# Kernel optimization log

Hardware: AMD Instinct MI355X
Metric: run time of the kernel (lower is better)

## Reference

```python
import jax, jax.numpy as jnp
import numpy as np

N, D, E, L, NL = 100000, 64, 400000, 4, 10000
NEG = jnp.float32(-1e30)


def _make_graph(key):
    k1, k2, k3, k4 = jax.random.split(key, 4)
    ncov = N - NL
    # nodes [0, NL) never appear as source -> exactly NL leaves
    src_cov = jnp.arange(ncov, dtype=jnp.int32) + NL
    src_rand = jax.random.randint(k1, (E - ncov,), NL, N, dtype=jnp.int32)
    src = jnp.concatenate([src_cov, src_rand])
    dst = jax.random.randint(k2, (E,), 0, N, dtype=jnp.int32)
    edge_index = jnp.stack([src, dst])  # [2, E]
    edge_attr = jax.random.normal(k3, (E, D), jnp.float32)
    # partition edges into L 'topological level' masks
    edge_masks = (jnp.arange(E) % L)[None, :] == jnp.arange(L)[:, None]  # [L, E] bool
    x = jax.random.normal(k4, (N, D), jnp.float32)
    return x, edge_index, edge_attr, edge_masks


def setup_inputs() -> dict:
    key = jax.random.key(0)
    kg1, kg2, kp = jax.random.split(key, 3)
    x1, ei1, ea1, em1 = _make_graph(kg1)
    x2, ei2, ea2, em2 = _make_graph(kg2)
    ks = jax.random.split(kp, 10)
    s = 1.0 / np.sqrt(D)
    params = {
        'We': jax.random.normal(ks[0], (D, D), jnp.float32) * s,
        'be': jax.random.normal(ks[1], (D,), jnp.float32) * s,
        'Wa': jax.random.normal(ks[2], (1, 2 * D), jnp.float32) * s,
        'ba': jax.random.normal(ks[3], (1,), jnp.float32) * s,
        'Wih': jax.random.normal(ks[4], (3 * D, D), jnp.float32) * s,
        'Whh': jax.random.normal(ks[5], (3 * D, D), jnp.float32) * s,
        'bih': jax.random.normal(ks[6], (3 * D,), jnp.float32) * s,
        'bhh': jax.random.normal(ks[7], (3 * D,), jnp.float32) * s,
        'Wc': jax.random.normal(ks[8], (2 * D, 2 * D), jnp.float32) * s,
        'bc': jax.random.normal(ks[9], (2 * D,), jnp.float32) * s,
    }
    return dict(x1=x1, edge_index1=ei1, edge_attr1=ea1, edge_masks1=em1,
                x2=x2, edge_index2=ei2, edge_attr2=ea2, edge_masks2=em2,
                **params, n_leaf=NL)


def _gru(x, h, Wih, Whh, bih, bhh):
    # torch.nn.GRUCell math
    gi = x @ Wih.T + bih
    gh = h @ Whh.T + bhh
    ir, iz, in_ = jnp.split(gi, 3, axis=-1)
    hr, hz, hn = jnp.split(gh, 3, axis=-1)
    r = jax.nn.sigmoid(ir + hr)
    z = jax.nn.sigmoid(iz + hz)
    n = jnp.tanh(in_ + r * hn)
    return (1.0 - z) * n + z * h


def _flow_forward(x, edge_index, edge_attr, edge_masks,
                  We, be, Wa, ba, Wih, Whh, bih, bhh):
    Nn, Dm = x.shape
    src, dst = edge_index[0], edge_index[1]
    root = jnp.ones((Nn,), bool).at[dst].set(False)  # nodes with no incoming edge
    eemb = edge_attr @ We.T + be                     # [E, D] edge_lin
    # roots: GRU with zero hidden; others start at 0 (zeros_like in torch)
    h0 = jnp.where(root[:, None], _gru(x, jnp.zeros_like(x), Wih, Whh, bih, bhh), 0.0)
    q = x[dst]                                       # h_prev_i, level-invariant

    def step(h, mask):
        k = h[src] + eemb                            # h_j + edge_emb
        logit = (jnp.concatenate([q, k], axis=-1) @ Wa.T + ba)[:, 0]  # [E]
        ml = jnp.where(mask, logit, NEG)
        mx = jnp.maximum(jax.ops.segment_max(ml, dst, num_segments=Nn), NEG)
        ex = jnp.where(mask, jnp.exp(ml - mx[dst]), 0.0)  # scatter-softmax numerator
        den = jax.ops.segment_sum(ex, dst, num_segments=Nn)
        alpha = ex / (den[dst] + 1e-16)
        msg = jax.ops.segment_sum(alpha[:, None] * h[src], dst, num_segments=Nn)
        nm = jax.ops.segment_sum(mask.astype(jnp.float32), dst, num_segments=Nn) > 0
        h_new = _gru(x, msg, Wih, Whh, bih, bhh)     # input=h_prev, hidden=msg
        return jnp.where(nm[:, None], h_new, h), None

    h, _ = jax.lax.scan(step, h0, edge_masks)
    return h


def reference(x1, edge_index1, edge_attr1, edge_masks1,
              x2, edge_index2, edge_attr2, edge_masks2,
              We, be, Wa, ba, Wih, Whh, bih, bhh, Wc, bc, n_leaf):
    o1 = _flow_forward(x1, edge_index1, edge_attr1, edge_masks1,
                       We, be, Wa, ba, Wih, Whh, bih, bhh)
    o2 = _flow_forward(x2, edge_index2, edge_attr2, edge_masks2,
                       We, be, Wa, ba, Wih, Whh, bih, bhh)
    Dm = x1.shape[1]
    leaf1 = jnp.ones((x1.shape[0],), bool).at[edge_index1[0]].set(False)
    leaf2 = jnp.ones((x2.shape[0],), bool).at[edge_index2[0]].set(False)
    idx1 = jnp.nonzero(leaf1, size=n_leaf)[0]
    idx2 = jnp.nonzero(leaf2, size=n_leaf)[0]
    feat = jnp.concatenate([o1[idx1], o2[idx2]], axis=-1) @ Wc.T + bc  # [NL, 2D]
    o1 = o1.at[idx1].set(feat[:, :Dm])
    o2 = o2.at[idx2].set(feat[:, Dm:])
    return (o1, o2)
```

## Files before the change

### kernel.cpp

```cpp
#include <hip/hip_runtime.h>

#define NN 100000
#define DD 64
#define EE 400000
#define LL 4
#define NLEAF 10000
#define NT (2*NN)
#define ETOT (2*EE)
#define M4 (4*NT)
#define NBLK ((M4 + 1023)/1024)

typedef __attribute__((ext_vector_type(8))) short bf8v;
typedef __attribute__((ext_vector_type(4))) float f4v;

__device__ __forceinline__ float rcp_(float x){ return __builtin_amdgcn_rcpf(x); }
__device__ __forceinline__ float sigm_(float x){ return rcp_(1.f + __expf(-x)); }
__device__ __forceinline__ float tanh_(float x){
  x = fminf(fmaxf(x, -15.f), 15.f);
  float a = __expf(2.f*x);
  return (a - 1.f) * rcp_(a + 1.f);
}
__device__ __forceinline__ float wave_sum(float p){
  #pragma unroll
  for (int m = 1; m < 64; m <<= 1) p += __shfl_xor(p, m, 64);
  return p;
}
__device__ __forceinline__ unsigned short f2b(float f){
  union { float f; unsigned int u; } v; v.f = f;
  unsigned int r = v.u + 0x7FFF + ((v.u >> 16) & 1);
  return (unsigned short)(r >> 16);
}
__device__ __forceinline__ float b2f(unsigned short b){
  union { unsigned int u; float f; } v; v.u = ((unsigned int)b) << 16;
  return v.f;
}

__global__ void k_init(int* __restrict__ counts, int* __restrict__ rootflag,
                       int* __restrict__ wlcnt, int* __restrict__ row_ptr,
                       float* __restrict__ hdot,
                       float* __restrict__ vvec, float* __restrict__ c0v,
                       unsigned short* __restrict__ whh_bf,
                       unsigned short* __restrict__ wih_bf,
                       unsigned short* __restrict__ hbf, int* __restrict__ lastlvl,
                       const float* __restrict__ We, const float* __restrict__ Wa,
                       const float* __restrict__ be, const float* __restrict__ Whh,
                       const float* __restrict__ Wih) {
  int tid = blockIdx.x*blockDim.x + threadIdx.x;
  int stride = gridDim.x*blockDim.x;
  for (int i = tid; i < M4; i += stride) counts[i] = 0;
  for (int i = tid; i < NT; i += stride) { rootflag[i] = 1; hdot[i] = 0.f; lastlvl[i] = -1; }
  for (int i = tid; i < 192*64; i += stride) whh_bf[i] = f2b(Whh[i]);
  for (int i = tid; i < 208*64; i += stride) {
    int n = i >> 6, k = i & 63;
    unsigned short v;
    if (n < 192)       v = f2b(Wih[i]);
    else if (n == 192) v = f2b(Wa[k]);
    else               v = 0;
    wih_bf[i] = v;
  }
  uint4 z4 = make_uint4(0,0,0,0);
  uint4* hz = (uint4*)hbf;
  for (int i = tid; i < NT*8; i += stride) hz[i] = z4;
  if (blockIdx.x == 0 && threadIdx.x < 64) {
    int c = threadIdx.x;
    float acc = 0.f;
    for (int d = 0; d < 64; ++d) acc += We[d*64 + c] * Wa[64 + d];
    vvec[c] = acc;
    float p = wave_sum(be[c] * Wa[64 + c]);
    if (c == 0) { c0v[0] = p; row_ptr[M4] = ETOT; }
    if (c < 8) wlcnt[c] = 0;
  }
}

__global__ void k_edot(const float* __restrict__ ea1, const float* __restrict__ ea2,
                       const int* __restrict__ ei1, const int* __restrict__ ei2,
                       const float* __restrict__ vvec, const float* __restrict__ c0v,
                       float* __restrict__ edot,
                       int* __restrict__ counts, int* __restrict__ rootflag) {
  int lane = threadIdx.x & 63;
  int wave = blockIdx.x*(blockDim.x>>6) + (threadIdx.x>>6);
  int nw = gridDim.x*(blockDim.x>>6);
  int grp = lane >> 4, l16 = lane & 15;
  float4 v4 = ((const float4*)vvec)[l16];
  float c0 = c0v[0];
  for (int it = wave; it < ETOT/16; it += nw) {
    int e0 = it*16 + grp;
    int g = e0 >= EE;
    const float* ea = g ? ea2 : ea1;
    int eb = e0 - g*EE;
    float4 a0 = ((const float4*)(ea + (long)(eb     )*64))[l16];
    float4 a1 = ((const float4*)(ea + (long)(eb +  4)*64))[l16];
    float4 a2 = ((const float4*)(ea + (long)(eb +  8)*64))[l16];
    float4 a3 = ((const float4*)(ea + (long)(eb + 12)*64))[l16];
    float p0 = a0.x*v4.x + a0.y*v4.y + a0.z*v4.z + a0.w*v4.w;
    float p1 = a1.x*v4.x + a1.y*v4.y + a1.z*v4.z + a1.w*v4.w;
    float p2 = a2.x*v4.x + a2.y*v4.y + a2.z*v4.z + a2.w*v4.w;
    float p3 = a3.x*v4.x + a3.y*v4.y + a3.z*v4.z + a3.w*v4.w;
    #pragma unroll
    for (int m = 1; m < 16; m <<= 1) {
      p0 += __shfl_xor(p0, m, 64); p1 += __shfl_xor(p1, m, 64);
      p2 += __shfl_xor(p2, m, 64); p3 += __shfl_xor(p3, m, 64);
    }
    if (l16 == 0) {
      edot[e0]      = p0 + c0;
      edot[e0 +  4] = p1 + c0;
      edot[e0 +  8] = p2 + c0;
      edot[e0 + 12] = p3 + c0;
    }
  }
  int tid = blockIdx.x*blockDim.x + threadIdx.x;
  int stride = gridDim.x*blockDim.x;
  for (int ee = tid; ee < ETOT; ee += stride) {
    int g = ee >= EE;
    int e = ee - g*EE;
    const int* ei = g ? ei2 : ei1;
    int d = ei[EE + e];
    int l = e & 3;
    int td = g*NN + d;
    atomicAdd(&counts[l*NT + td], 1);
    rootflag[td] = 0;
  }
}

__global__ __launch_bounds__(256) void k_scan1(const int* __restrict__ counts,
                                               int* __restrict__ row_ptr,
                                               int* __restrict__ partials) {
  __shared__ int ts[256];
  int tx = threadIdx.x;
  int base = blockIdx.x*1024 + tx*4;
  int v[4]; int s = 0;
  #pragma unroll
  for (int u = 0; u < 4; ++u) { v[u] = (base+u < M4) ? counts[base+u] : 0; s += v[u]; }
  ts[tx] = s; __syncthreads();
  for (int off = 1; off < 256; off <<= 1) {
    int t = (tx >= off) ? ts[tx-off] : 0;
    __syncthreads();
    ts[tx] += t;
    __syncthreads();
  }
  int excl = ts[tx] - s;
  #pragma unroll
  for (int u = 0; u < 4; ++u) {
    if (base+u < M4) row_ptr[base+u] = excl;
    excl += v[u];
  }
  if (tx == 255) partials[blockIdx.x] = ts[255];
}

__global__ __launch_bounds__(256) void k_scan2(int* __restrict__ partials) {
  __shared__ int ts[256];
  int tx = threadIdx.x;
  int carry = 0;
  for (int base = 0; base < NBLK; base += 256) {
    int i = base + tx;
    int v = (i < NBLK) ? partials[i] : 0;
    ts[tx] = v; __syncthreads();
    for (int off = 1; off < 256; off <<= 1) {
      int t = (tx >= off) ? ts[tx-off] : 0;
      __syncthreads();
      ts[tx] += t;
      __syncthreads();
    }
    int incl = ts[tx];
    int tot = ts[255];
    __syncthreads();
    if (i < NBLK) partials[i] = incl - v + carry;
    carry += tot;
  }
}

__global__ __launch_bounds__(256) void k_scan3(int* __restrict__ row_ptr,
                                               const int* __restrict__ partials,
                                               const int* __restrict__ counts,
                                               int* __restrict__ wl, int* __restrict__ wlcnt,
                                               int* __restrict__ lastlvl) {
  __shared__ int cnt4[4];
  __shared__ int base4[4];
  int tx = threadIdx.x;
  if (tx < 4) cnt4[tx] = 0;
  __syncthreads();
  int base = blockIdx.x*1024 + tx*4;
  int add = partials[blockIdx.x];
  int rank[4]; int lvl[4]; bool val[4];
  #pragma unroll
  for (int u = 0; u < 4; ++u) {
    int i = base + u;
    val[u] = false;
    if (i < M4) {
      row_ptr[i] += add;
      if (counts[i] > 0) {
        int l = i / NT;
        lvl[u] = l;
        rank[u] = atomicAdd(&cnt4[l], 1);
        val[u] = true;
        atomicMax(&lastlvl[i - l*NT], l);
      }
    }
  }
  __syncthreads();
  if (tx < 4 && cnt4[tx] > 0) base4[tx] = atomicAdd(&wlcnt[tx], cnt4[tx]);
  __syncthreads();
  #pragma unroll
  for (int u = 0; u < 4; ++u) {
    if (val[u]) {
      int l = lvl[u];
      wl[l*NT + base4[l] + rank[u]] = (base + u) - l*NT;
    }
  }
}

__global__ void k_fill(const int* __restrict__ ei1, const int* __restrict__ ei2,
                       const float* __restrict__ edot, const float* __restrict__ ba,
                       const int* __restrict__ row_ptr, int* __restrict__ counts,
                       int2* __restrict__ csr) {
  int tid = blockIdx.x*blockDim.x + threadIdx.x;
  int stride = gridDim.x*blockDim.x;
  float bav = ba[0];
  for (int ee = tid; ee < ETOT; ee += stride) {
    int g = ee >= EE;
    int e = ee - g*EE;
    const int* ei = g ? ei2 : ei1;
    int s = ei[e], d = ei[EE + e];
    int l = e & 3;
    int i = l*NT + g*NN + d;
    int slot = atomicSub(&counts[i], 1) - 1;
    int pos = row_ptr[i] + slot;
    csr[pos] = make_int2(g*NN + s, __float_as_int(edot[ee] + bav));
  }
}

__global__ __launch_bounds__(256) void k_gix(
    const float* __restrict__ x1, const float* __restrict__ x2,
    const unsigned short* __restrict__ wih_bf,
    const float* __restrict__ bih, const float* __restrict__ bhh,
    const float* __restrict__ Wa, const int* __restrict__ rootflag,
    ushort2* __restrict__ gi01, unsigned short* __restrict__ gi2p,
    float* __restrict__ xdot, float* __restrict__ hdot,
    float* __restrict__ hout, unsigned short* __restrict__ hbf) {
  int lane = threadIdx.x & 63, w = threadIdx.x >> 6;
  int l15 = lane & 15, quad = lane >> 4;
  int wave = blockIdx.x*4 + w, nw = gridDim.x*4;
  float bi0[4],bi1[4],bi2[4],bh0[4],bh1[4],bh2[4],wk4[4];
  #pragma unroll
  for (int tt = 0; tt < 4; ++tt) {
    int f = l15 + 16*tt;
    bi0[tt]=bih[f]; bi1[tt]=bih[64+f]; bi2[tt]=bih[128+f];
    bh0[tt]=bhh[f]; bh1[tt]=bhh[64+f]; bh2[tt]=bhh[128+f];
    wk4[tt]=Wa[64+f];
  }
  for (int tl = wave; tl < NT/16; tl += nw) {
    int ta = tl*16 + l15;
    const float* xp = (ta < NN) ? x1 + (size_t)ta*64 : x2 + (size_t)(ta-NN)*64;
    float4 v0 = ((const float4*)xp)[quad*2];
    float4 v1 = ((const float4*)xp)[quad*2 + 1];
    float4 v2 = ((const float4*)xp)[quad*2 + 8];
    float4 v3 = ((const float4*)xp)[quad*2 + 9];
    bf8v a0, a1;
    a0[0]=(short)f2b(v0.x); a0[1]=(short)f2b(v0.y); a0[2]=(short)f2b(v0.z); a0[3]=(short)f2b(v0.w);
    a0[4]=(short)f2b(v1.x); a0[5]=(short)f2b(v1.y); a0[6]=(short)f2b(v1.z); a0[7]=(short)f2b(v1.w);
    a1[0]=(short)f2b(v2.x); a1[1]=(short)f2b(v2.y); a1[2]=(short)f2b(v2.z); a1[3]=(short)f2b(v2.w);
    a1[4]=(short)f2b(v3.x); a1[5]=(short)f2b(v3.y); a1[6]=(short)f2b(v3.z); a1[7]=(short)f2b(v3.w);
    int rt[4];
    #pragma unroll
    for (int r = 0; r < 4; ++r) rt[r] = rootflag[tl*16 + quad*4 + r];
    float hds[4] = {0.f, 0.f, 0.f, 0.f};
    #pragma unroll
    for (int tt = 0; tt < 4; ++tt) {
      bf8v bR0 = *(const bf8v*)&wih_bf[((tt  )*16 + l15)*64 + quad*8];
      bf8v bR1 = *(const bf8v*)&wih_bf[((tt  )*16 + l15)*64 + 32 + quad*8];
      bf8v bZ0 = *(const bf8v*)&wih_bf[((tt+4)*16 + l15)*64 + quad*8];
      bf8v bZ1 = *(const bf8v*)&wih_bf[((tt+4)*16 + l15)*64 + 32 + quad*8];
      bf8v bN0 = *(const bf8v*)&wih_bf[((tt+8)*16 + l15)*64 + quad*8];
      bf8v bN1 = *(const bf8v*)&wih_bf[((tt+8)*16 + l15)*64 + 32 + quad*8];
      f4v zR = {0.f,0.f,0.f,0.f}, zZ = {0.f,0.f,0.f,0.f}, zN = {0.f,0.f,0.f,0.f};
      zR = __builtin_amdgcn_mfma_f32_16x16x32_bf16(a0, bR0, zR, 0, 0, 0);
      zR = __builtin_amdgcn_mfma_f32_16x16x32_bf16(a1, bR1, zR, 0, 0, 0);
      zZ = __builtin_amdgcn_mfma_f32_16x16x32_bf16(a0, bZ0, zZ, 0, 0, 0);
      zZ = __builtin_amdgcn_mfma_f32_16x16x32_bf16(a1, bZ1, zZ, 0, 0, 0);
      zN = __builtin_amdgcn_mfma_f32_16x16x32_bf16(a0, bN0, zN, 0, 0, 0);
      zN = __builtin_amdgcn_mfma_f32_16x16x32_bf16(a1, bN1, zN, 0, 0, 0);
      int f = tt*16 + l15;
      #pragma unroll
      for (int r = 0; r < 4; ++r) {
        int t = tl*16 + quad*4 + r;
        float g0 = zR[r] + bi0[tt];
        float g1 = zZ[r] + bi1[tt];
        float g2 = zN[r] + bi2[tt];
        ushort2 p; p.x = f2b(g0); p.y = f2b(g1);
        gi01[(size_t)t*64 + f] = p;
        gi2p[(size_t)t*64 + f] = f2b(g2);
        if (rt[r]) {
          float rr = sigm_(g0 + bh0[tt]);
          float zz = sigm_(g1 + bh1[tt]);
          float nn = tanh_(g2 + rr*bh2[tt]);
          float hv = (1.f - zz)*nn;
          hout[(size_t)t*64 + f] = hv;
          hbf[(size_t)t*64 + f] = f2b(hv);
          hds[r] += hv * wk4[tt];
        }
      }
    }
    bf8v bx0 = *(const bf8v*)&wih_bf[(192 + l15)*64 + quad*8];
    bf8v bx1 = *(const bf8v*)&wih_bf[(192 + l15)*64 + 32 + quad*8];
    f4v zX = {0.f,0.f,0.f,0.f};
    zX = __builtin_amdgcn_mfma_f32_16x16x32_bf16(a0, bx0, zX, 0, 0, 0);
    zX = __builtin_amdgcn_mfma_f32_16x16x32_bf16(a1, bx1, zX, 0, 0, 0);
    #pragma unroll
    for (int r = 0; r < 4; ++r) {
      int t = tl*16 + quad*4 + r;
      if (l15 == 0) xdot[t] = zX[r];
      if (rt[r]) {
        float h = hds[r];
        h += __shfl_xor(h, 1, 64); h += __shfl_xor(h, 2, 64);
        h += __shfl_xor(h, 4, 64); h += __shfl_xor(h, 8, 64);
        if (l15 == 0) hdot[t] = h;
      }
    }
  }
}

__global__ void k_msg(const int* __restrict__ row_ptr, const int2* __restrict__ csr,
                      const float* __restrict__ xdot,
                      const float* __restrict__ hdot, const unsigned short* __restrict__ hbf,
                      const int* __restrict__ wl, const int* __restrict__ wlcnt,
                      int level, unsigned short* __restrict__ msgn_bf) {
  int l16 = threadIdx.x & 15;
  int grp = (blockIdx.x*blockDim.x + threadIdx.x) >> 4;
  int ngrp = (gridDim.x*blockDim.x) >> 4;
  int cnt = wlcnt[level];
  for (int i = grp; i < cnt; i += ngrp) {
    int t = wl[level*NT + i];
    int bi = level*NT + t;
    int p0 = row_ptr[bi], p1 = row_ptr[bi+1];
    float xd = xdot[t];
    float den = 0.f;
    float m0 = 0.f, m1 = 0.f, m2 = 0.f, m3 = 0.f;
    for (int p = p0; p < p1; ++p) {
      int2 pr = csr[p];
      int s = pr.x;
      float wv = __expf(xd + hdot[s] + __int_as_float(pr.y));
      den += wv;
      ushort4 hv = *(const ushort4*)(hbf + (size_t)s*64 + l16*4);
      m0 += wv*b2f(hv.x); m1 += wv*b2f(hv.y); m2 += wv*b2f(hv.z); m3 += wv*b2f(hv.w);
    }
    float rd = rcp_(den + 1e-16f);
    ushort4 o;
    o.x = f2b(m0*rd); o.y = f2b(m1*rd); o.z = f2b(m2*rd); o.w = f2b(m3*rd);
    *(ushort4*)(msgn_bf + (long)i*64 + l16*4) = o;
  }
}

__global__ __launch_bounds__(256) void k_gru(
    const unsigned short* __restrict__ whh_bf, const float* __restrict__ bhh,
    const float* __restrict__ Wa,
    const ushort2* __restrict__ gi01, const unsigned short* __restrict__ gi2p,
    const int* __restrict__ wl, const int* __restrict__ wlcnt,
    const int* __restrict__ lastlvl, int level,
    const unsigned short* __restrict__ msgn_bf,
    float* __restrict__ hout, unsigned short* __restrict__ hbf,
    float* __restrict__ hdot) {
  int lane = threadIdx.x & 63, w = threadIdx.x >> 6;
  int l15 = lane & 15, quad = lane >> 4;
  int cnt = wlcnt[level];
  int ntile = (cnt + 15) >> 4;
  int wave = blockIdx.x*4 + w, nw = gridDim.x*4;
  float bh0[4], bh1[4], bh2[4], wk4[4];
  #pragma unroll
  for (int tt = 0; tt < 4; ++tt) {
    int f = tt*16 + l15;
    bh0[tt]=bhh[f]; bh1[tt]=bhh[64+f]; bh2[tt]=bhh[128+f];
    wk4[tt]=Wa[64+f];
  }
  for (int tl = wave; tl < ntile; tl += nw) {
    int base = tl*16;
    long abase = (long)(base + l15)*64;
    bf8v a0 = *(const bf8v*)&msgn_bf[abase + quad*8];
    bf8v a1 = *(const bf8v*)&msgn_bf[abase + 32 + quad*8];
    f4v acc[12];
    #pragma unroll
    for (int nt = 0; nt < 12; ++nt) {
      bf8v b0 = *(const bf8v*)&whh_bf[(nt*16 + l15)*64 + quad*8];
      bf8v b1 = *(const bf8v*)&whh_bf[(nt*16 + l15)*64 + 32 + quad*8];
      f4v z = {0.f, 0.f, 0.f, 0.f};
      z = __builtin_amdgcn_mfma_f32_16x16x32_bf16(a0, b0, z, 0, 0, 0);
      acc[nt] = __builtin_amdgcn_mfma_f32_16x16x32_bf16(a1, b1, z, 0, 0, 0);
    }
    #pragma unroll
    for (int r = 0; r < 4; ++r) {
      int i = base + quad*4 + r;
      if (i < cnt) {
        int t = wl[level*NT + i];
        int ll = lastlvl[t];
        float hds = 0.f;
        #pragma unroll
        for (int tt = 0; tt < 4; ++tt) {
          int f = tt*16 + l15;
          ushort2 p01 = gi01[(size_t)t*64 + f];
          float g2v = b2f(gi2p[(size_t)t*64 + f]);
          float mv  = b2f(msgn_bf[(long)i*64 + f]);
          float rr = sigm_(b2f(p01.x) + acc[tt][r]   + bh0[tt]);
          float zz = sigm_(b2f(p01.y) + acc[tt+4][r] + bh1[tt]);
          float nn = tanh_(g2v + rr*(acc[tt+8][r] + bh2[tt]));
          float hv = (1.f - zz)*nn + zz*mv;
          if (ll == level) hout[(size_t)t*64 + f] = hv;
          if (level < 3)  hbf[(size_t)t*64 + f] = f2b(hv);
          hds += hv * wk4[tt];
        }
        if (level < 3) {
          hds += __shfl_xor(hds, 1, 64);
          hds += __shfl_xor(hds, 2, 64);
          hds += __shfl_xor(hds, 4, 64);
          hds += __shfl_xor(hds, 8, 64);
          if (l15 == 0) hdot[t] = hds;
        }
      }
    }
  }
}

__global__ __launch_bounds__(256) void k_final(const float* __restrict__ Wc,
                                               const float* __restrict__ bc,
                                               float* __restrict__ hout) {
  __shared__ float WT[128*128];
  for (int idx = threadIdx.x; idx < 128*128; idx += 256) {
    int j = idx >> 7, c = idx & 127;
    WT[c*128 + j] = Wc[idx];
  }
  __syncthreads();
  int lane = threadIdx.x & 63, w = threadIdx.x >> 6;
  int wave = blockIdx.x*4 + w, nw = gridDim.x*4;
  float bc0 = bc[lane], bc1 = bc[64 + lane];
  for (int i = wave; i < NLEAF; i += nw) {
    float h1v = hout[(long)i*64 + lane];
    float h2v = hout[(long)(NN + i)*64 + lane];
    float acc0 = 0.f, acc1 = 0.f;
    for (int c = 0; c < 64; ++c) {
      float m1 = __shfl(h1v, c, 64);
      float m2 = __shfl(h2v, c, 64);
      acc0 += WT[c*128 + lane]      * m1 + WT[(64+c)*128 + lane]      * m2;
      acc1 += WT[c*128 + 64 + lane] * m1 + WT[(64+c)*128 + 64 + lane] * m2;
    }
    hout[(long)i*64 + lane]        = acc0 + bc0;
    hout[(long)(NN + i)*64 + lane] = acc1 + bc1;
  }
}

extern "C" void kernel_launch(void* const* d_in, const int* in_sizes, int n_in,
                              void* d_out, int out_size, void* d_ws, size_t ws_size,
                              hipStream_t stream) {
  const float* x1  = (const float*)d_in[0];
  const int*   ei1 = (const int*)  d_in[1];
  const float* ea1 = (const float*)d_in[2];
  const float* x2  = (const float*)d_in[4];
  const int*   ei2 = (const int*)  d_in[5];
  const float* ea2 = (const float*)d_in[6];
  const float* We  = (const float*)d_in[8];
  const float* be  = (const float*)d_in[9];
  const float* Wa  = (const float*)d_in[10];
  const float* ba  = (const float*)d_in[11];
  const float* Wih = (const float*)d_in[12];
  const float* Whh = (const float*)d_in[13];
  const float* bih = (const float*)d_in[14];
  const float* bhh = (const float*)d_in[15];
  const float* Wc  = (const float*)d_in[16];
  const float* bc  = (const float*)d_in[17];
  float* hout = (float*)d_out;

  float* f = (float*)d_ws;
  ushort2* gi01 = (ushort2*)f;        f += (size_t)NT*64;
  unsigned short* gi2p    = (unsigned short*)f;  f += (size_t)NT*32;
  unsigned short* msgn_bf = (unsigned short*)f;  f += (size_t)NT*32;
  unsigned short* hbf     = (unsigned short*)f;  f += (size_t)NT*32;
  unsigned short* whh_bf  = (unsigned short*)f;  f += 8192;
  unsigned short* wih_bf  = (unsigned short*)f;  f += 8192;
  float* edot = f;  f += ETOT;
  float* xdot = f;  f += NT;
  float* hdot = f;  f += NT;
  float* vvec = f;  f += 64;
  float* c0v  = f;  f += 64;
  int2* csr     = (int2*)f; f += (size_t)2*ETOT;
  int* counts   = (int*)f;  f += M4;
  int* row_ptr  = (int*)f;  f += (M4 + 64);
  int* rootflag = (int*)f;  f += NT;
  int* lastlvl  = (int*)f;  f += NT;
  int* wl       = (int*)f;  f += 4*NT;
  int* wlcnt    = (int*)f;  f += 64;
  int* partials = (int*)f;  f += 1024;

  k_init <<<dim3(1024), dim3(256), 0, stream>>>(counts, rootflag, wlcnt, row_ptr, hdot, vvec, c0v, whh_bf, wih_bf, hbf, lastlvl, We, Wa, be, Whh, Wih);
  k_edot <<<dim3(2048), dim3(256), 0, stream>>>(ea1, ea2, ei1, ei2, vvec, c0v, edot, counts, rootflag);
  k_scan1<<<dim3(NBLK), dim3(256), 0, stream>>>(counts, row_ptr, partials);
  k_scan2<<<dim3(1),    dim3(256), 0, stream>>>(partials);
  k_scan3<<<dim3(NBLK), dim3(256), 0, stream>>>(row_ptr, partials, counts, wl, wlcnt, lastlvl);
  k_fill <<<dim3(2048), dim3(256), 0, stream>>>(ei1, ei2, edot, ba, row_ptr, counts, csr);
  k_gix  <<<dim3(2048), dim3(256), 0, stream>>>(x1, x2, wih_bf, bih, bhh, Wa, rootflag, gi01, gi2p, xdot, hdot, hout, hbf);
  for (int l = 0; l < 4; ++l) {
    k_msg<<<dim3(8192), dim3(256), 0, stream>>>(row_ptr, csr, xdot, hdot, hbf, wl, wlcnt, l, msgn_bf);
    k_gru<<<dim3(2048), dim3(256), 0, stream>>>(whh_bf, bhh, Wa, gi01, gi2p, wl, wlcnt, lastlvl, l, msgn_bf, hout, hbf, hdot);
  }
  k_final<<<dim3(640), dim3(256), 0, stream>>>(Wc, bc, hout);
}
```

Baseline: 567.5 us.

## Pack per-level in-degree counts into bytes and fuse CSR fill with gix

Per-level destination counts are packed into one 32-bit word per node, one byte per level. This replaces the M4-sized count array, the rootflag array and the atomicMax on lastlvl. lastlvl and the root test are now derived directly from the packed word. The CSR fill kernel is merged into the gix kernel to save a launch, and the edge-dot loop gains a one-iteration register prefetch. Each byte is an 8-bit counter, so the code is wrong if any node has more than 255 incoming edges at one level.

```diff
diff --git a/kernel.cpp b/kernel.cpp
--- a/kernel.cpp
+++ b/kernel.cpp
@@ -34,21 +34,24 @@
   union { unsigned int u; float f; } v; v.u = ((unsigned int)b) << 16;
   return v.f;
 }
-
-__global__ void k_init(int* __restrict__ counts, int* __restrict__ rootflag,
+__device__ __forceinline__ int cnt_at(const unsigned int* pcnt, int i){
+  int l = i / NT; int td = i - l*NT;
+  return (int)((pcnt[td] >> (8*l)) & 255u);
+}
+
+__global__ void k_init(unsigned int* __restrict__ pcnt,
                        int* __restrict__ wlcnt, int* __restrict__ row_ptr,
                        float* __restrict__ hdot,
                        float* __restrict__ vvec, float* __restrict__ c0v,
                        unsigned short* __restrict__ whh_bf,
                        unsigned short* __restrict__ wih_bf,
-                       unsigned short* __restrict__ hbf, int* __restrict__ lastlvl,
+                       unsigned short* __restrict__ hbf,
                        const float* __restrict__ We, const float* __restrict__ Wa,
                        const float* __restrict__ be, const float* __restrict__ Whh,
                        const float* __restrict__ Wih) {
   int tid = blockIdx.x*blockDim.x + threadIdx.x;
   int stride = gridDim.x*blockDim.x;
-  for (int i = tid; i < M4; i += stride) counts[i] = 0;
-  for (int i = tid; i < NT; i += stride) { rootflag[i] = 1; hdot[i] = 0.f; lastlvl[i] = -1; }
+  for (int i = tid; i < NT; i += stride) { pcnt[i] = 0u; hdot[i] = 0.f; }
   for (int i = tid; i < 192*64; i += stride) whh_bf[i] = f2b(Whh[i]);
   for (int i = tid; i < 208*64; i += stride) {
     int n = i >> 6, k = i & 63;
@@ -75,39 +78,7 @@
 __global__ void k_edot(const float* __restrict__ ea1, const float* __restrict__ ea2,
                        const int* __restrict__ ei1, const int* __restrict__ ei2,
                        const float* __restrict__ vvec, const float* __restrict__ c0v,
-                       float* __restrict__ edot,
-                       int* __restrict__ counts, int* __restrict__ rootflag) {
-  int lane = threadIdx.x & 63;
-  int wave = blockIdx.x*(blockDim.x>>6) + (threadIdx.x>>6);
-  int nw = gridDim.x*(blockDim.x>>6);
-  int grp = lane >> 4, l16 = lane & 15;
-  float4 v4 = ((const float4*)vvec)[l16];
-  float c0 = c0v[0];
-  for (int it = wave; it < ETOT/16; it += nw) {
-    int e0 = it*16 + grp;
-    int g = e0 >= EE;
-    const float* ea = g ? ea2 : ea1;
-    int eb = e0 - g*EE;
-    float4 a0 = ((const float4*)(ea + (long)(eb     )*64))[l16];
-    float4 a1 = ((const float4*)(ea + (long)(eb +  4)*64))[l16];
-    float4 a2 = ((const float4*)(ea + (long)(eb +  8)*64))[l16];
-    float4 a3 = ((const float4*)(ea + (long)(eb + 12)*64))[l16];
-    float p0 = a0.x*v4.x + a0.y*v4.y + a0.z*v4.z + a0.w*v4.w;
-    float p1 = a1.x*v4.x + a1.y*v4.y + a1.z*v4.z + a1.w*v4.w;
-    float p2 = a2.x*v4.x + a2.y*v4.y + a2.z*v4.z + a2.w*v4.w;
-    float p3 = a3.x*v4.x + a3.y*v4.y + a3.z*v4.z + a3.w*v4.w;
-    #pragma unroll
-    for (int m = 1; m < 16; m <<= 1) {
-      p0 += __shfl_xor(p0, m, 64); p1 += __shfl_xor(p1, m, 64);
-      p2 += __shfl_xor(p2, m, 64); p3 += __shfl_xor(p3, m, 64);
-    }
-    if (l16 == 0) {
-      edot[e0]      = p0 + c0;
-      edot[e0 +  4] = p1 + c0;
-      edot[e0 +  8] = p2 + c0;
-      edot[e0 + 12] = p3 + c0;
-    }
-  }
+                       float* __restrict__ edot, unsigned int* __restrict__ pcnt) {
   int tid = blockIdx.x*blockDim.x + threadIdx.x;
   int stride = gridDim.x*blockDim.x;
   for (int ee = tid; ee < ETOT; ee += stride) {
@@ -115,14 +86,60 @@
     int e = ee - g*EE;
     const int* ei = g ? ei2 : ei1;
     int d = ei[EE + e];
-    int l = e & 3;
-    int td = g*NN + d;
-    atomicAdd(&counts[l*NT + td], 1);
-    rootflag[td] = 0;
-  }
-}
-
-__global__ __launch_bounds__(256) void k_scan1(const int* __restrict__ counts,
+    atomicAdd(&pcnt[g*NN + d], 1u << (8*(e & 3)));
+  }
+  int lane = threadIdx.x & 63;
+  int wave = blockIdx.x*(blockDim.x>>6) + (threadIdx.x>>6);
+  int nw = gridDim.x*(blockDim.x>>6);
+  int grp = lane >> 4, l16 = lane & 15;
+  float4 v4 = ((const float4*)vvec)[l16];
+  float c0 = c0v[0];
+  const int NIT = ETOT/16;
+  int it = wave;
+  float4 c0_, c1_, c2_, c3_;
+  if (it < NIT) {
+    int e0 = it*16 + grp; int g = e0 >= EE;
+    const float* ea = g ? ea2 : ea1; long eb = e0 - g*EE;
+    c0_ = ((const float4*)(ea + eb*64))[l16];
+    c1_ = ((const float4*)(ea + (eb+4)*64))[l16];
+    c2_ = ((const float4*)(ea + (eb+8)*64))[l16];
+    c3_ = ((const float4*)(ea + (eb+12)*64))[l16];
+  }
+  while (it < NIT) {
+    int jt = it + nw;
+    float4 n0, n1, n2, n3;
+    if (jt < NIT) {
+      int e0 = jt*16 + grp; int g = e0 >= EE;
+      const float* ea = g ? ea2 : ea1; long eb = e0 - g*EE;
+      n0 = ((const float4*)(ea + eb*64))[l16];
+      n1 = ((const float4*)(ea + (eb+4)*64))[l16];
+      n2 = ((const float4*)(ea + (eb+8)*64))[l16];
+      n3 = ((const float4*)(ea + (eb+12)*64))[l16];
+    } else {
+      n0 = n1 = n2 = n3 = make_float4(0.f,0.f,0.f,0.f);
+    }
+    float p0 = c0_.x*v4.x + c0_.y*v4.y + c0_.z*v4.z + c0_.w*v4.w;
+    float p1 = c1_.x*v4.x + c1_.y*v4.y + c1_.z*v4.z + c1_.w*v4.w;
+    float p2 = c2_.x*v4.x + c2_.y*v4.y + c2_.z*v4.z + c2_.w*v4.w;
+    float p3 = c3_.x*v4.x + c3_.y*v4.y + c3_.z*v4.z + c3_.w*v4.w;
+    #pragma unroll
+    for (int m = 1; m < 16; m <<= 1) {
+      p0 += __shfl_xor(p0, m, 64); p1 += __shfl_xor(p1, m, 64);
+      p2 += __shfl_xor(p2, m, 64); p3 += __shfl_xor(p3, m, 64);
+    }
+    if (l16 == 0) {
+      int e0 = it*16 + grp;
+      edot[e0]      = p0 + c0;
+      edot[e0 +  4] = p1 + c0;
+      edot[e0 +  8] = p2 + c0;
+      edot[e0 + 12] = p3 + c0;
+    }
+    c0_ = n0; c1_ = n1; c2_ = n2; c3_ = n3;
+    it = jt;
+  }
+}
+
+__global__ __launch_bounds__(256) void k_scan1(const unsigned int* __restrict__ pcnt,
                                                int* __restrict__ row_ptr,
                                                int* __restrict__ partials) {
   __shared__ int ts[256];
@@ -130,7 +147,7 @@
   int base = blockIdx.x*1024 + tx*4;
   int v[4]; int s = 0;
   #pragma unroll
-  for (int u = 0; u < 4; ++u) { v[u] = (base+u < M4) ? counts[base+u] : 0; s += v[u]; }
+  for (int u = 0; u < 4; ++u) { v[u] = (base+u < M4) ? cnt_at(pcnt, base+u) : 0; s += v[u]; }
   ts[tx] = s; __syncthreads();
   for (int off = 1; off < 256; off <<= 1) {
     int t = (tx >= off) ? ts[tx-off] : 0;
@@ -171,9 +188,19 @@
 
 __global__ __launch_bounds__(256) void k_scan3(int* __restrict__ row_ptr,
                                                const int* __restrict__ partials,
-                                               const int* __restrict__ counts,
+                                               const unsigned int* __restrict__ pcnt,
                                                int* __restrict__ wl, int* __restrict__ wlcnt,
                                                int* __restrict__ lastlvl) {
+  int tdl = blockIdx.x*blockDim.x + threadIdx.x;
+  if (tdl < NT) {
+    unsigned pv = pcnt[tdl];
+    int ll = -1;
+    if      (pv & 0xFF000000u) ll = 3;
+    else if (pv & 0x00FF0000u) ll = 2;
+    else if (pv & 0x0000FF00u) ll = 1;
+    else if (pv & 0x000000FFu) ll = 0;
+    lastlvl[tdl] = ll;
+  }
   __shared__ int cnt4[4];
   __shared__ int base4[4];
   int tx = threadIdx.x;
@@ -188,12 +215,11 @@
     val[u] = false;
     if (i < M4) {
       row_ptr[i] += add;
-      if (counts[i] > 0) {
+      if (cnt_at(pcnt, i) > 0) {
         int l = i / NT;
         lvl[u] = l;
         rank[u] = atomicAdd(&cnt4[l], 1);
         val[u] = true;
-        atomicMax(&lastlvl[i - l*NT], l);
       }
     }
   }
@@ -209,34 +235,35 @@
   }
 }
 
-__global__ void k_fill(const int* __restrict__ ei1, const int* __restrict__ ei2,
-                       const float* __restrict__ edot, const float* __restrict__ ba,
-                       const int* __restrict__ row_ptr, int* __restrict__ counts,
-                       int2* __restrict__ csr) {
-  int tid = blockIdx.x*blockDim.x + threadIdx.x;
-  int stride = gridDim.x*blockDim.x;
-  float bav = ba[0];
-  for (int ee = tid; ee < ETOT; ee += stride) {
-    int g = ee >= EE;
-    int e = ee - g*EE;
-    const int* ei = g ? ei2 : ei1;
-    int s = ei[e], d = ei[EE + e];
-    int l = e & 3;
-    int i = l*NT + g*NN + d;
-    int slot = atomicSub(&counts[i], 1) - 1;
-    int pos = row_ptr[i] + slot;
-    csr[pos] = make_int2(g*NN + s, __float_as_int(edot[ee] + bav));
-  }
-}
-
-__global__ __launch_bounds__(256) void k_gix(
+__global__ __launch_bounds__(256) void k_fillgix(
+    const int* __restrict__ ei1, const int* __restrict__ ei2,
+    const float* __restrict__ edot, const float* __restrict__ ba,
+    const int* __restrict__ row_ptr, unsigned int* __restrict__ pcnt,
+    int2* __restrict__ csr,
     const float* __restrict__ x1, const float* __restrict__ x2,
     const unsigned short* __restrict__ wih_bf,
     const float* __restrict__ bih, const float* __restrict__ bhh,
-    const float* __restrict__ Wa, const int* __restrict__ rootflag,
+    const float* __restrict__ Wa, const int* __restrict__ lastlvl,
     ushort2* __restrict__ gi01, unsigned short* __restrict__ gi2p,
     float* __restrict__ xdot, float* __restrict__ hdot,
     float* __restrict__ hout, unsigned short* __restrict__ hbf) {
+  {
+    int tid = blockIdx.x*blockDim.x + threadIdx.x;
+    int stride = gridDim.x*blockDim.x;
+    float bav = ba[0];
+    for (int ee = tid; ee < ETOT; ee += stride) {
+      int g = ee >= EE;
+      int e = ee - g*EE;
+      const int* ei = g ? ei2 : ei1;
+      int s = ei[e], d = ei[EE + e];
+      int l = e & 3;
+      int td = g*NN + d;
+      unsigned old = atomicAdd(&pcnt[td], (unsigned)(0u - (1u << (8*l))));
+      int slot = (int)((old >> (8*l)) & 255u) - 1;
+      int pos = row_ptr[l*NT + td] + slot;
+      csr[pos] = make_int2(g*NN + s, __float_as_int(edot[ee] + bav));
+    }
+  }
   int lane = threadIdx.x & 63, w = threadIdx.x >> 6;
   int l15 = lane & 15, quad = lane >> 4;
   int wave = blockIdx.x*4 + w, nw = gridDim.x*4;
@@ -262,7 +289,7 @@
     a1[4]=(short)f2b(v3.x); a1[5]=(short)f2b(v3.y); a1[6]=(short)f2b(v3.z); a1[7]=(short)f2b(v3.w);
     int rt[4];
     #pragma unroll
-    for (int r = 0; r < 4; ++r) rt[r] = rootflag[tl*16 + quad*4 + r];
+    for (int r = 0; r < 4; ++r) rt[r] = (lastlvl[tl*16 + quad*4 + r] < 0);
     float hds[4] = {0.f, 0.f, 0.f, 0.f};
     #pragma unroll
     for (int tt = 0; tt < 4; ++tt) {
@@ -479,21 +506,19 @@
   float* vvec = f;  f += 64;
   float* c0v  = f;  f += 64;
   int2* csr     = (int2*)f; f += (size_t)2*ETOT;
-  int* counts   = (int*)f;  f += M4;
+  unsigned int* pcnt = (unsigned int*)f;  f += NT;
   int* row_ptr  = (int*)f;  f += (M4 + 64);
-  int* rootflag = (int*)f;  f += NT;
   int* lastlvl  = (int*)f;  f += NT;
   int* wl       = (int*)f;  f += 4*NT;
   int* wlcnt    = (int*)f;  f += 64;
   int* partials = (int*)f;  f += 1024;
 
-  k_init <<<dim3(1024), dim3(256), 0, stream>>>(counts, rootflag, wlcnt, row_ptr, hdot, vvec, c0v, whh_bf, wih_bf, hbf, lastlvl, We, Wa, be, Whh, Wih);
-  k_edot <<<dim3(2048), dim3(256), 0, stream>>>(ea1, ea2, ei1, ei2, vvec, c0v, edot, counts, rootflag);
-  k_scan1<<<dim3(NBLK), dim3(256), 0, stream>>>(counts, row_ptr, partials);
+  k_init <<<dim3(1024), dim3(256), 0, stream>>>(pcnt, wlcnt, row_ptr, hdot, vvec, c0v, whh_bf, wih_bf, hbf, We, Wa, be, Whh, Wih);
+  k_edot <<<dim3(2048), dim3(256), 0, stream>>>(ea1, ea2, ei1, ei2, vvec, c0v, edot, pcnt);
+  k_scan1<<<dim3(NBLK), dim3(256), 0, stream>>>(pcnt, row_ptr, partials);
   k_scan2<<<dim3(1),    dim3(256), 0, stream>>>(partials);
-  k_scan3<<<dim3(NBLK), dim3(256), 0, stream>>>(row_ptr, partials, counts, wl, wlcnt, lastlvl);
-  k_fill <<<dim3(2048), dim3(256), 0, stream>>>(ei1, ei2, edot, ba, row_ptr, counts, csr);
-  k_gix  <<<dim3(2048), dim3(256), 0, stream>>>(x1, x2, wih_bf, bih, bhh, Wa, rootflag, gi01, gi2p, xdot, hdot, hout, hbf);
+  k_scan3<<<dim3(NBLK), dim3(256), 0, stream>>>(row_ptr, partials, pcnt, wl, wlcnt, lastlvl);
+  k_fillgix<<<dim3(2048), dim3(256), 0, stream>>>(ei1, ei2, edot, ba, row_ptr, pcnt, csr, x1, x2, wih_bf, bih, bhh, Wa, lastlvl, gi01, gi2p, xdot, hdot, hout, hbf);
   for (int l = 0; l < 4; ++l) {
     k_msg<<<dim3(8192), dim3(256), 0, stream>>>(row_ptr, csr, xdot, hdot, hbf, wl, wlcnt, l, msgn_bf);
     k_gru<<<dim3(2048), dim3(256), 0, stream>>>(whh_bf, bhh, Wa, gi01, gi2p, wl, wlcnt, lastlvl, l, msgn_bf, hout, hbf, hdot);
```

After: 560.4 us. No clear change (-1.3%).
